# Optimization experiments

Hardware: AMD Instinct MI355X
Metric: run time of the kernel (lower is better)

## Reference

```python
import jax, jax.numpy as jnp
import numpy as np

HIDDEN = 2048
INTER = 8192  # shard == INTER since world_size == 1
BATCH, LOCAL_SEQ = 2, 4096


def setup_inputs() -> dict:
    key = jax.random.key(0)
    k1, k2, k3 = jax.random.split(key, 3)
    h_shard = jax.random.normal(k1, (BATCH, LOCAL_SEQ, HIDDEN), dtype=jnp.float32)
    # torch Linear weights are [out_features, in_features]
    w_gate_up = jax.random.normal(k2, (2 * INTER, HIDDEN), dtype=jnp.float32) * 0.02
    w_down = jax.random.normal(k3, (HIDDEN, INTER), dtype=jnp.float32) * 0.02
    return {"h_shard": h_shard, "w_gate_up": w_gate_up, "w_down": w_down}


def reference(h_shard, w_gate_up, w_down):
    # world_size == 1: ag_mm == matmul (all-gather is identity),
    # mm_rs == matmul (reduce-scatter of single partial is identity).
    batch, local_seq, hidden = h_shard.shape
    # gate_up: [b, s, 2*shard]
    gate_up = jnp.einsum('bsh,oh->bso', h_shard, w_gate_up)
    gate, up = jnp.split(gate_up, 2, axis=-1)
    h = jax.nn.silu(gate) * up  # [b, s, shard]
    out = jnp.einsum('bsi,hi->bsh', h, w_down)  # [b, s, hidden]
    return out
```

## Files before the change

### kernel.cpp

```cpp
#include <hip/hip_runtime.h>
#include <hip/hip_bf16.h>
#include <cstdint>
#include <cstddef>

#define HIDDEN 2048
#define INTER 8192
#define M_TOK 8192

typedef __attribute__((ext_vector_type(8))) short short8;
typedef __attribute__((ext_vector_type(4))) float float4v;

typedef __hip_bfloat16 bf16;

__global__ void cvt_bf16(const float* __restrict__ src, bf16* __restrict__ dst, int n) {
    int idx = blockIdx.x * blockDim.x + threadIdx.x;
    int stride = gridDim.x * blockDim.x;
    for (int i = idx * 4; i < n; i += stride * 4) {
        float4 v = *(const float4*)(src + i);
        union { bf16 h[4]; ushort4 u; } pk;
        pk.h[0] = __float2bfloat16(v.x);
        pk.h[1] = __float2bfloat16(v.y);
        pk.h[2] = __float2bfloat16(v.z);
        pk.h[3] = __float2bfloat16(v.w);
        *(ushort4*)(dst + i) = pk.u;
    }
}

__device__ __forceinline__ void load16_lds(const bf16* g, bf16* l) {
    __builtin_amdgcn_global_load_lds((const __attribute__((address_space(1))) void*)g,
                                     (__attribute__((address_space(3))) void*)l,
                                     16, 0, 0);
}

template<int KDIM, bool FUSE>
__global__ __launch_bounds__(512, 2) void gemm_8ph(const bf16* __restrict__ A,
                                                   const bf16* __restrict__ B,
                                                   bf16* __restrict__ actout,
                                                   float* __restrict__ cout) {
    static_assert(KDIM % 64 == 0, "KDIM multiple of 64");
    __shared__ __align__(16) bf16 sm[2 * 32768];

    constexpr int NKT = KDIM / 64;

    const int tid  = threadIdx.x;
    const int wave = tid >> 6;
    const int lane = tid & 63;
    const int wm = wave >> 2;
    const int wn = wave & 3;
    const int lm = lane & 15;
    const int kg = lane >> 4;

    const int m0 = blockIdx.y * 256;
    const int n0 = blockIdx.x * (FUSE ? 128 : 256);

    const int srow = wave * 8 + (lane >> 3);
    const int scol = ((lane & 7) ^ (lane >> 3)) * 8;
    const bf16* ag[4];
    const bf16* bg[4];
#pragma unroll
    for (int q = 0; q < 4; ++q) {
        const int arow = m0 + (q & 1) * 128 + (q >> 1) * 64 + srow;
        ag[q] = A + (size_t)arow * KDIM + scol;
        int brow;
        if (FUSE) {
            brow = n0 + (q >> 1) * (INTER - 128) + q * 64 + srow;
        } else {
            const int t = (q & 1) * 64 + srow;
            brow = n0 + (t >> 5) * 64 + (q >> 1) * 32 + (t & 31);
        }
        bg[q] = B + (size_t)brow * KDIM + scol;
    }
    bf16* const sdA = sm + wave * 512;
    bf16* const sdB = sm + 16384 + wave * 512;

    const int sl0 = ((0 * 4 + kg) ^ (lm & 7)) * 8;
    const int sl1 = ((1 * 4 + kg) ^ (lm & 7)) * 8;

    float4v acc[8][4];
#pragma unroll
    for (int i = 0; i < 8; i++)
#pragma unroll
        for (int j = 0; j < 4; j++) acc[i][j] = (float4v)0.f;

    short8 af[8];
    short8 bq[4];
    short8 bq2[4];

#define STAGE_A(h, nb, kn) { \
        load16_lds(ag[(h)*2+0] + (size_t)(kn)*64, sdA + (nb)*32768 + ((h)*2+0)*4096); \
        load16_lds(ag[(h)*2+1] + (size_t)(kn)*64, sdA + (nb)*32768 + ((h)*2+1)*4096); }
#define STAGE_B(h, nb, kn) { \
        load16_lds(bg[(h)*2+0] + (size_t)(kn)*64, sdB + (nb)*32768 + ((h)*2+0)*4096); \
        load16_lds(bg[(h)*2+1] + (size_t)(kn)*64, sdB + (nb)*32768 + ((h)*2+1)*4096); }
#define LOAD_A(dst, ih, smA_) { \
        _Pragma("unroll") \
        for (int i2 = 0; i2 < 4; i2++) { \
            const bf16* p = (smA_) + ((ih) * 128 + wm * 64 + i2 * 16 + lm) * 64; \
            dst[i2*2+0] = *(const short8*)(p + sl0); \
            dst[i2*2+1] = *(const short8*)(p + sl1); } }
#define LOAD_B(dst, jh, smB_) { \
        _Pragma("unroll") \
        for (int j2 = 0; j2 < 2; j2++) { \
            const bf16* p = (smB_) + ((jh) * 128 + wn * 32 + j2 * 16 + lm) * 64; \
            dst[j2*2+0] = *(const short8*)(p + sl0); \
            dst[j2*2+1] = *(const short8*)(p + sl1); } }
#define MFMA_Q(A_, B_, ih, jh) { \
        _Pragma("unroll") \
        for (int i2 = 0; i2 < 4; i2++) \
        _Pragma("unroll") \
        for (int j2 = 0; j2 < 2; j2++) { \
            acc[(ih)*4+i2][(jh)*2+j2] = __builtin_amdgcn_mfma_f32_16x16x32_bf16(A_[i2*2+0], B_[j2*2+0], acc[(ih)*4+i2][(jh)*2+j2], 0, 0, 0); \
            acc[(ih)*4+i2][(jh)*2+j2] = __builtin_amdgcn_mfma_f32_16x16x32_bf16(A_[i2*2+1], B_[j2*2+1], acc[(ih)*4+i2][(jh)*2+j2], 0, 0, 0); } }
#define FENCE asm volatile("" ::: "memory")
#define BAR   do { FENCE; __builtin_amdgcn_s_barrier(); FENCE; } while (0)

    STAGE_A(0, 0, 0);
    STAGE_B(0, 0, 0);
    STAGE_B(1, 0, 0);
    STAGE_A(1, 0, 0);
    asm volatile("s_waitcnt vmcnt(4)" ::: "memory");
    BAR;

    for (int kt = 0; kt < NKT; ++kt) {
        const int bb = kt & 1;
        const int nb = bb ^ 1;
        const int kn = (kt + 1 < NKT) ? (kt + 1) : 0;
        const bf16* smA = sm + bb * 32768;
        const bf16* smB = smA + 16384;

        STAGE_A(0, nb, kn);
        LOAD_A(af, 0, smA);
        LOAD_B(bq, 0, smB);
        asm volatile("s_waitcnt vmcnt(4)" ::: "memory");
        BAR;
        __builtin_amdgcn_s_setprio(1);
        MFMA_Q(af, bq, 0, 0);
        __builtin_amdgcn_s_setprio(0);
        __builtin_amdgcn_sched_barrier(0);

        STAGE_B(0, nb, kn);
        LOAD_B(bq2, 1, smB);
        asm volatile("s_waitcnt vmcnt(4)" ::: "memory");
        BAR;
        __builtin_amdgcn_s_setprio(1);
        MFMA_Q(af, bq2, 0, 1);
        __builtin_amdgcn_s_setprio(0);
        __builtin_amdgcn_sched_barrier(0);

        STAGE_B(1, nb, kn);
        LOAD_A(af, 1, smA);
        BAR;
        __builtin_amdgcn_s_setprio(1);
        MFMA_Q(af, bq2, 1, 1);
        __builtin_amdgcn_s_setprio(0);
        __builtin_amdgcn_sched_barrier(0);

        STAGE_A(1, nb, kn);
        asm volatile("s_waitcnt vmcnt(4)" ::: "memory");
        BAR;
        __builtin_amdgcn_s_setprio(1);
        MFMA_Q(af, bq, 1, 0);
        __builtin_amdgcn_s_setprio(0);
        __builtin_amdgcn_sched_barrier(0);
    }
    asm volatile("s_waitcnt vmcnt(0)" ::: "memory");

    if (FUSE) {
        const int orow = m0 + wm * 128;
        const int ocol = n0 + wn * 32;
#pragma unroll
        for (int i = 0; i < 8; i++)
#pragma unroll
            for (int j2 = 0; j2 < 2; j2++)
#pragma unroll
                for (int r = 0; r < 4; r++) {
                    const float g = acc[i][j2][r];
                    const float u = acc[i][j2 + 2][r];
                    const float a = (g / (1.f + __expf(-g))) * u;
                    actout[(size_t)(orow + i * 16 + kg * 4 + r) * INTER + ocol + j2 * 16 + lm] =
                        __float2bfloat16(a);
                }
    } else {
        const int orow = m0 + wm * 128;
        const int ocol = n0 + wn * 64;
#pragma unroll
        for (int i = 0; i < 8; i++)
#pragma unroll
            for (int j = 0; j < 4; j++)
#pragma unroll
                for (int r = 0; r < 4; r++)
                    cout[(size_t)(orow + i * 16 + kg * 4 + r) * HIDDEN + ocol + j * 16 + lm] =
                        acc[i][j][r];
    }
#undef STAGE_A
#undef STAGE_B
#undef LOAD_A
#undef LOAD_B
#undef MFMA_Q
#undef FENCE
#undef BAR
}

extern "C" void kernel_launch(void* const* d_in, const int* in_sizes, int n_in,
                              void* d_out, int out_size, void* d_ws, size_t ws_size,
                              hipStream_t stream) {
    const float* h   = (const float*)d_in[0];
    const float* wgu = (const float*)d_in[1];
    const float* wd  = (const float*)d_in[2];
    float* out = (float*)d_out;

    char* ws = (char*)d_ws;
    bf16* hbf   = (bf16*)(ws);
    bf16* wgubf = (bf16*)(ws + 33554432ull);
    bf16* wdbf  = (bf16*)(ws + 100663296ull);
    bf16* actbf = (bf16*)(ws + 134217728ull);

    cvt_bf16<<<dim3(4096), 256, 0, stream>>>(h,   hbf,   M_TOK * HIDDEN);
    cvt_bf16<<<dim3(8192), 256, 0, stream>>>(wgu, wgubf, 2 * INTER * HIDDEN);
    cvt_bf16<<<dim3(4096), 256, 0, stream>>>(wd,  wdbf,  HIDDEN * INTER);

    gemm_8ph<HIDDEN, true><<<dim3(64, 32), 512, 0, stream>>>(hbf, wgubf, actbf, nullptr);

    gemm_8ph<INTER, false><<<dim3(8, 32), 512, 0, stream>>>(actbf, wdbf, nullptr, out);
}
```

Baseline: 952.9 us.

## Prefetch LDS fragments one phase ahead and swizzle block-to-tile mapping

Each LDS fragment read now sits right after the preceding MFMA phase instead of after the barrier that guards the MFMAs that use it. The first A/B fragments of the next k-tile are read at the end of the current iteration from the other buffer. The intent is to hide LDS read latency behind MFMA work, at the cost of more live registers and an extra vmcnt wait in the third phase. Block indices are also remapped into groups of 4 M-tiles by consecutive N-tiles, to improve L2 reuse of A and B tiles across concurrently running workgroups.

```diff
diff --git a/kernel.cpp b/kernel.cpp
--- a/kernel.cpp
+++ b/kernel.cpp
@@ -50,8 +50,13 @@
     const int lm = lane & 15;
     const int kg = lane >> 4;
 
-    const int m0 = blockIdx.y * 256;
-    const int n0 = blockIdx.x * (FUSE ? 128 : 256);
+    const int id = blockIdx.y * gridDim.x + blockIdx.x;
+    const int w_ = id >> 3;
+    const int by = (id & 7) * 4 + (w_ & 3);
+    const int bx = w_ >> 2;
+
+    const int m0 = by * 256;
+    const int n0 = bx * (FUSE ? 128 : 256);
 
     const int srow = wave * 8 + (lane >> 3);
     const int scol = ((lane & 7) ^ (lane >> 3)) * 8;
@@ -113,55 +118,62 @@
             acc[(ih)*4+i2][(jh)*2+j2] = __builtin_amdgcn_mfma_f32_16x16x32_bf16(A_[i2*2+1], B_[j2*2+1], acc[(ih)*4+i2][(jh)*2+j2], 0, 0, 0); } }
 #define FENCE asm volatile("" ::: "memory")
 #define BAR   do { FENCE; __builtin_amdgcn_s_barrier(); FENCE; } while (0)
+#define VMC4  asm volatile("s_waitcnt vmcnt(4)" ::: "memory")
+#define SBAR0 __builtin_amdgcn_sched_barrier(0)
 
     STAGE_A(0, 0, 0);
     STAGE_B(0, 0, 0);
     STAGE_B(1, 0, 0);
     STAGE_A(1, 0, 0);
-    asm volatile("s_waitcnt vmcnt(4)" ::: "memory");
+    VMC4;
     BAR;
+    LOAD_A(af, 0, sm);
+    LOAD_B(bq, 0, sm + 16384);
 
     for (int kt = 0; kt < NKT; ++kt) {
         const int bb = kt & 1;
         const int nb = bb ^ 1;
         const int kn = (kt + 1 < NKT) ? (kt + 1) : 0;
-        const bf16* smA = sm + bb * 32768;
-        const bf16* smB = smA + 16384;
+        const bf16* smA  = sm + bb * 32768;
+        const bf16* smB  = smA + 16384;
+        const bf16* smA2 = sm + nb * 32768;
+        const bf16* smB2 = smA2 + 16384;
 
         STAGE_A(0, nb, kn);
-        LOAD_A(af, 0, smA);
-        LOAD_B(bq, 0, smB);
-        asm volatile("s_waitcnt vmcnt(4)" ::: "memory");
+        VMC4;
         BAR;
         __builtin_amdgcn_s_setprio(1);
         MFMA_Q(af, bq, 0, 0);
         __builtin_amdgcn_s_setprio(0);
-        __builtin_amdgcn_sched_barrier(0);
+        SBAR0;
+        LOAD_B(bq2, 1, smB);
 
         STAGE_B(0, nb, kn);
-        LOAD_B(bq2, 1, smB);
-        asm volatile("s_waitcnt vmcnt(4)" ::: "memory");
+        VMC4;
         BAR;
         __builtin_amdgcn_s_setprio(1);
         MFMA_Q(af, bq2, 0, 1);
         __builtin_amdgcn_s_setprio(0);
-        __builtin_amdgcn_sched_barrier(0);
+        SBAR0;
+        LOAD_A(af, 1, smA);
 
         STAGE_B(1, nb, kn);
-        LOAD_A(af, 1, smA);
+        VMC4;
         BAR;
         __builtin_amdgcn_s_setprio(1);
         MFMA_Q(af, bq2, 1, 1);
         __builtin_amdgcn_s_setprio(0);
-        __builtin_amdgcn_sched_barrier(0);
+        SBAR0;
 
         STAGE_A(1, nb, kn);
-        asm volatile("s_waitcnt vmcnt(4)" ::: "memory");
+        VMC4;
         BAR;
         __builtin_amdgcn_s_setprio(1);
         MFMA_Q(af, bq, 1, 0);
         __builtin_amdgcn_s_setprio(0);
-        __builtin_amdgcn_sched_barrier(0);
+        SBAR0;
+        LOAD_A(af, 0, smA2);
+        LOAD_B(bq, 0, smB2);
     }
     asm volatile("s_waitcnt vmcnt(0)" ::: "memory");
 
@@ -199,6 +211,8 @@
 #undef MFMA_Q
 #undef FENCE
 #undef BAR
+#undef VMC4
+#undef SBAR0
 }
 
 extern "C" void kernel_launch(void* const* d_in, const int* in_sizes, int n_in,
```

Result: faster. 932.4 us (-2.2%).
